# Optimization experiments

Measured on AMD Instinct MI355X. Metric: run time of the kernel, lower is better.

## Reference

```python
import jax, jax.numpy as jnp
import numpy as np

B, N, M = 2, 2048, 2048
D_K, D_V, H = 256, 256, 8
D_KS = D_K // H  # 32, per-head key dim (ceil(256/8))
D_VS = D_V // H  # 32
MASK_BIG = 1e32


def setup_inputs() -> dict:
    key = jax.random.key(0)
    ks = jax.random.split(key, 10)
    s = 0.02
    queries = jax.random.normal(ks[0], (B, N, D_K), jnp.float32)
    keys_ = jax.random.normal(ks[1], (B, M, D_K), jnp.float32)
    values = jax.random.normal(ks[2], (B, M, D_V), jnp.float32)
    presence = (jax.random.uniform(ks[3], (B, M)) > 0.3).astype(jnp.float32)
    Wq = jax.random.normal(ks[4], (D_K, D_KS * H), jnp.float32) * s
    bq = jnp.zeros((D_KS * H,), jnp.float32)
    Wk = jax.random.normal(ks[5], (D_K, D_KS * H), jnp.float32) * s
    bk = jnp.zeros((D_KS * H,), jnp.float32)
    Wv = jax.random.normal(ks[6], (D_V, D_VS * H), jnp.float32) * s
    bv = jnp.zeros((D_VS * H,), jnp.float32)
    Wo = jax.random.normal(ks[7], (D_VS * H, D_V), jnp.float32) * s
    bo = jnp.zeros((D_V,), jnp.float32)
    return {"queries": queries, "keys": keys_, "values": values, "presence": presence,
            "Wq": Wq, "bq": bq, "Wk": Wk, "bk": bk, "Wv": Wv, "bv": bv, "Wo": Wo, "bo": bo}


def reference(queries, keys, values, presence, Wq, bq, Wk, bk, Wv, bv, Wo, bo):
    # Project and split into heads. torch's split(d_k_s,-1)+cat(...,0) puts the
    # head index as the outer batch dim; a [B,N,H,d] reshape is the same math.
    q = (queries @ Wq + bq).reshape(B, N, H, D_KS)
    k = (keys @ Wk + bk).reshape(B, M, H, D_KS)
    v = (values @ Wv + bv).reshape(B, M, H, D_VS)
    # Raw scores, additive presence mask, then scale by sqrt(per-head d_k)
    scores = jnp.einsum('bnhd,bmhd->bhnm', q, k)
    scores = scores - (1.0 - presence)[:, None, None, :] * MASK_BIG
    attn = jax.nn.softmax(scores / np.sqrt(D_KS).astype(np.float32), axis=-1)
    o = jnp.einsum('bhnm,bmhd->bnhd', attn, v).reshape(B, N, H * D_VS)
    return o @ Wo + bo
```

## Files before the change

### kernel.cpp

```cpp
#include <hip/hip_runtime.h>

#define B_ 2
#define N_ 2048
#define M_ 2048
#define D_ 256
#define H_ 8
#define DH_ 32
#define SPLITS 2
#define QSCALE (0.17677669529663689f * 1.4426950408889634f)

typedef __attribute__((ext_vector_type(8))) short short8;
typedef __attribute__((ext_vector_type(4))) float f32x4;
typedef unsigned short u16;
typedef unsigned int u32;

#if __has_builtin(__builtin_amdgcn_exp2f)
#define EXP2 __builtin_amdgcn_exp2f
#else
#define EXP2 exp2f
#endif

__device__ __forceinline__ u16 f2bf(float f) {
  u32 u = __float_as_uint(f);
  return (u16)((u + 0x7fffu + ((u >> 16) & 1u)) >> 16);
}
__device__ __forceinline__ u32 cvtpk_bf16(float lo, float hi) {
  u32 r;
  asm("v_cvt_pk_bf16_f32 %0, %1, %2" : "=v"(r) : "v"(lo), "v"(hi));
  return r;
}
__device__ __forceinline__ void gload_lds16(const u16* g, u16* l) {
  __builtin_amdgcn_global_load_lds((const __attribute__((address_space(1))) void*)g,
                                   (__attribute__((address_space(3))) void*)l, 16, 0, 0);
}
__device__ __forceinline__ void gload_lds16f(const float* g, float* l) {
  __builtin_amdgcn_global_load_lds((const __attribute__((address_space(1))) void*)g,
                                   (__attribute__((address_space(3))) void*)l, 16, 0, 0);
}

__global__ __launch_bounds__(256) void wtconv_kernel(
    const float* __restrict__ Wq, const float* __restrict__ Wk,
    const float* __restrict__ Wv, const float* __restrict__ Wo,
    u16* __restrict__ wTq, u16* __restrict__ wTk, u16* __restrict__ wTv,
    u16* __restrict__ wTo) {
  __shared__ u16 sh[64][72];
  const int blk = blockIdx.x;
  const int mi = blk >> 4, tile = blk & 15;
  const float* Ws = mi == 0 ? Wq : mi == 1 ? Wk : mi == 2 ? Wv : Wo;
  u16* Wd = mi == 0 ? wTq : mi == 1 ? wTk : mi == 2 ? wTv : wTo;
  const int r0 = (tile >> 2) * 64, c0 = (tile & 3) * 64;
  const int r = threadIdx.x & 63, qt = threadIdx.x >> 6;
  const float* sp = Ws + (size_t)(r0 + r) * D_ + c0 + qt * 16;
  u32 w[8];
#pragma unroll
  for (int i = 0; i < 4; ++i) {
    f32x4 v = *(const f32x4*)(sp + i * 4);
    w[i * 2 + 0] = cvtpk_bf16(v[0], v[1]);
    w[i * 2 + 1] = cvtpk_bf16(v[2], v[3]);
  }
  *(uint4*)(&sh[r][qt * 16]) = *(uint4*)&w[0];
  *(uint4*)(&sh[r][qt * 16 + 8]) = *(uint4*)&w[4];
  __syncthreads();
  const int cc = threadIdx.x & 63;
  u32 t2[8];
#pragma unroll
  for (int i = 0; i < 8; ++i) {
    u32 lo = sh[qt * 16 + 2 * i][cc];
    u32 hi = sh[qt * 16 + 2 * i + 1][cc];
    t2[i] = lo | (hi << 16);
  }
  u16* op = Wd + (size_t)(c0 + cc) * D_ + r0 + qt * 16;
  *(uint4*)op = *(uint4*)&t2[0];
  *(uint4*)(op + 8) = *(uint4*)&t2[4];
}

__global__ __launch_bounds__(256, 4) void qkvproj_kernel(
    const float* __restrict__ Xq, const float* __restrict__ Xk, const float* __restrict__ Xv,
    const u16* __restrict__ wTq, const u16* __restrict__ wTk, const u16* __restrict__ wTv,
    const float* __restrict__ bq, const float* __restrict__ bk, const float* __restrict__ bv,
    u16* __restrict__ qb, u16* __restrict__ kb, u16* __restrict__ vtb) {
  __shared__ u16 xs[16 * 256];
  const int p = blockIdx.y;
  const int n0 = blockIdx.x * 16;
  const float* X = p == 0 ? Xq : (p == 1 ? Xk : Xv);
  const u16* wT = p == 0 ? wTq : (p == 1 ? wTk : wTv);
  const float* bias = p == 0 ? bq : (p == 1 ? bk : bv);
  const int t = threadIdx.x;

  {
    const int nL = t >> 4, kc = (t & 15) * 16;
    const float* xp = X + (size_t)(n0 + nL) * D_ + kc;
#pragma unroll
    for (int m = 0; m < 2; ++m) {
      const f32x4 a = *(const f32x4*)(xp + 8 * m);
      const f32x4 b2 = *(const f32x4*)(xp + 8 * m + 4);
      uint4 v;
      v.x = cvtpk_bf16(a[0], a[1]);
      v.y = cvtpk_bf16(a[2], a[3]);
      v.z = cvtpk_bf16(b2[0], b2[1]);
      v.w = cvtpk_bf16(b2[2], b2[3]);
      const int k0 = kc + 8 * m;
      *(uint4*)(xs + nL * 256 + (((k0 >> 3) ^ (nL & 7)) * 8)) = v;
    }
  }
  __syncthreads();

  const int wv = t >> 6, lane = t & 63, lr = lane & 15, lg = lane >> 4;
  const int c0 = wv * 64;
  const f32x4 zz = {0.f, 0.f, 0.f, 0.f};
  f32x4 acc[4] = {zz, zz, zz, zz};
#pragma unroll
  for (int ks = 0; ks < 8; ++ks) {
    const short8 a = *(const short8*)(xs + lr * 256 + (((ks * 4 + lg) ^ (lr & 7)) * 8));
#pragma unroll
    for (int ct = 0; ct < 4; ++ct) {
      const short8 b = *(const short8*)(wT + (size_t)(c0 + ct * 16 + lr) * D_ + ks * 32 + lg * 8);
      acc[ct] = __builtin_amdgcn_mfma_f32_16x16x32_bf16(a, b, acc[ct], 0, 0, 0);
    }
  }

  const int bidx = n0 >> 11;
  const int nn = (n0 & (N_ - 1)) + lg * 4;
  if (p < 2) {
    u16* ob = p == 0 ? qb : kb;
    const float sc = p == 0 ? QSCALE : 1.0f;
#pragma unroll
    for (int ct = 0; ct < 4; ++ct) {
      const int c = c0 + ct * 16 + lr;
      const float bb = bias[c];
      const int hh = c >> 5, dd = c & 31;
#pragma unroll
      for (int j = 0; j < 4; ++j)
        ob[((size_t)(bidx * H_ + hh) * N_ + nn + j) * DH_ + dd] =
            f2bf((acc[ct][j] + bb) * sc);
    }
  } else {
#pragma unroll
    for (int ct = 0; ct < 4; ++ct) {
      const int c = c0 + ct * 16 + lr;
      const float bb = bias[c];
      const int hh = c >> 5, dd = c & 31;
#pragma unroll
      for (int j = 0; j < 4; ++j)
        vtb[((size_t)(bidx * H_ + hh) * DH_ + dd) * M_ + nn + j] =
            f2bf(acc[ct][j] + bb);
    }
  }
}

__global__ __launch_bounds__(256, 4) void attn_kernel(
    const u16* __restrict__ qb, const u16* __restrict__ kb,
    const u16* __restrict__ vtb, const float* __restrict__ presence,
    float* __restrict__ opart, float* __restrict__ lpart) {
  __shared__ u16 kvlds[2][4096];
  __shared__ u16 plds[4][1024];
  __shared__ float prlds[1024];
  const int t = threadIdx.x;
  const int wv = t >> 6, lane = t & 63;
  const int lr = lane & 15, lg = lane >> 4;
  const int g = blockIdx.x;
  const int S = (g & 7) * 4 + ((g >> 3) & 3);
  const int qblk = g >> 5;
  const int s = S >> 4, bh = S & 15;
  const int b = bh >> 3, h = bh & 7;
  const int n0 = qblk * 64 + wv * 16;
  const int m0 = s * (M_ / SPLITS);
  const int NI = (M_ / SPLITS) / 64;

  const int gsk = (t & 3) ^ ((t >> 3) & 3);
  const u16* kst = kb + ((size_t)bh * M_ + m0 + (t >> 2)) * DH_ + gsk * 8;
  const int gsv = (t & 7) ^ ((t >> 3) & 7);
  const u16* vst = vtb + ((size_t)bh * DH_ + (t >> 3)) * M_ + m0 + gsv * 8;
  u16* const ldswK = &kvlds[0][0] + wv * 512;
  u16* const ldswV = &kvlds[0][0] + 2048 + wv * 512;

  const int ko0 = lr * 32 + (lg ^ ((lr >> 1) & 3)) * 8;
  const int sw = lr & 7;
  const int vo0 = (lg ^ sw) * 8;
  const int vo1 = ((4 + lg) ^ sw) * 8;

  const short8 qf = *(const short8*)(qb + ((size_t)bh * N_ + n0 + lr) * DH_ + lg * 8);
  u16* const plw = plds[wv] + lr * 64;

  const f32x4 zz = {0.f, 0.f, 0.f, 0.f};
  f32x4 o0 = zz, o1 = zz, racc = zz;

  gload_lds16(kst, ldswK);
  gload_lds16(vst, ldswV);
  gload_lds16f(presence + (size_t)b * M_ + m0 + wv * 256 + lane * 4, prlds + wv * 256);
  __syncthreads();

#pragma unroll 2
  for (int i = 0; i < NI; ++i) {
    const int mm = i * 64;
    const u16* kl = &kvlds[i & 1][0];
    const u16* vl = &kvlds[i & 1][2048];
    if (i + 1 < NI) {
      const int bo = ((i + 1) & 1) * 4096;
      gload_lds16(kst + (size_t)(i + 1) * (64 * DH_), ldswK + bo);
      gload_lds16(vst + (size_t)(i + 1) * 64, ldswV + bo);
    }

    f32x4 s4[4];
    __builtin_amdgcn_s_setprio(1);
#pragma unroll
    for (int tt = 0; tt < 4; ++tt) {
      const short8 kf = *(const short8*)(kl + tt * 512 + ko0);
      s4[tt] = __builtin_amdgcn_mfma_f32_16x16x32_bf16(kf, qf, zz, 0, 0, 0);
    }
    __builtin_amdgcn_s_setprio(0);

#pragma unroll
    for (int tt = 0; tt < 4; ++tt) {
      const f32x4 pr = *(const f32x4*)(prlds + mm + tt * 16 + lg * 4);
#pragma unroll
      for (int j = 0; j < 4; ++j) s4[tt][j] = EXP2(s4[tt][j]);
      s4[tt] *= pr;
      racc += s4[tt];
      const int slot = (2 * tt + (lg >> 1)) ^ sw;
      *(uint2*)(plw + slot * 8 + (lg & 1) * 4) =
          make_uint2(cvtpk_bf16(s4[tt][0], s4[tt][1]), cvtpk_bf16(s4[tt][2], s4[tt][3]));
    }
    const short8 pf0 = *(const short8*)(plw + vo0);
    const short8 pf1 = *(const short8*)(plw + vo1);
    const short8 vf0 = *(const short8*)(vl + lr * 64 + vo0);
    const short8 vf1 = *(const short8*)(vl + lr * 64 + vo1);
    const short8 vf2 = *(const short8*)(vl + (16 + lr) * 64 + vo0);
    const short8 vf3 = *(const short8*)(vl + (16 + lr) * 64 + vo1);
    __builtin_amdgcn_s_setprio(1);
    o0 = __builtin_amdgcn_mfma_f32_16x16x32_bf16(pf0, vf0, o0, 0, 0, 0);
    o0 = __builtin_amdgcn_mfma_f32_16x16x32_bf16(pf1, vf1, o0, 0, 0, 0);
    o1 = __builtin_amdgcn_mfma_f32_16x16x32_bf16(pf0, vf2, o1, 0, 0, 0);
    o1 = __builtin_amdgcn_mfma_f32_16x16x32_bf16(pf1, vf3, o1, 0, 0, 0);
    __builtin_amdgcn_s_setprio(0);
    __syncthreads();
  }

  float l = (racc[0] + racc[1]) + (racc[2] + racc[3]);
  l += __shfl_xor(l, 16);
  l += __shfl_xor(l, 32);
  if (lg == 0) lpart[((size_t)s * (B_ * N_) + b * N_ + n0 + lr) * H_ + h] = l;

  float* ob = opart + ((size_t)s * (B_ * N_) + (size_t)b * N_ + n0) * D_ + h * DH_;
#pragma unroll
  for (int j = 0; j < 4; ++j) {
    const int q = lg * 4 + j;
    ob[(size_t)q * D_ + lr] = o0[j];
    ob[(size_t)q * D_ + 16 + lr] = o1[j];
  }
}

__global__ __launch_bounds__(256, 4) void projo_kernel(
    const float* __restrict__ opart, const float* __restrict__ lpart,
    const u16* __restrict__ wTo, const float* __restrict__ bo,
    float* __restrict__ out) {
  __shared__ u16 xs[16 * 256];
  const int n0 = blockIdx.x * 16;
  const int t = threadIdx.x;

  {
    const int nL = t >> 4, kc = (t & 15) * 16;
    const int gn = n0 + nL;
    const float* o0p = opart + (size_t)gn * D_ + kc;
    const float* o1p = o0p + (size_t)(B_ * N_) * D_;
    const int h0 = kc >> 5;
    const float il = 1.f / (lpart[(size_t)gn * H_ + h0] +
                            lpart[((size_t)(B_ * N_) + gn) * H_ + h0]);
#pragma unroll
    for (int m = 0; m < 2; ++m) {
      f32x4 a = *(const f32x4*)(o0p + 8 * m) + *(const f32x4*)(o1p + 8 * m);
      f32x4 b2 = *(const f32x4*)(o0p + 8 * m + 4) + *(const f32x4*)(o1p + 8 * m + 4);
      a *= il;
      b2 *= il;
      uint4 v;
      v.x = cvtpk_bf16(a[0], a[1]);
      v.y = cvtpk_bf16(a[2], a[3]);
      v.z = cvtpk_bf16(b2[0], b2[1]);
      v.w = cvtpk_bf16(b2[2], b2[3]);
      const int k0 = kc + 8 * m;
      *(uint4*)(xs + nL * 256 + (((k0 >> 3) ^ (nL & 7)) * 8)) = v;
    }
  }
  __syncthreads();

  const int wv = t >> 6, lane = t & 63, lr = lane & 15, lg = lane >> 4;
  const int c0 = wv * 64;
  const f32x4 zz = {0.f, 0.f, 0.f, 0.f};
  f32x4 acc[4] = {zz, zz, zz, zz};
#pragma unroll
  for (int ks = 0; ks < 8; ++ks) {
    const short8 a = *(const short8*)(xs + lr * 256 + (((ks * 4 + lg) ^ (lr & 7)) * 8));
#pragma unroll
    for (int ct = 0; ct < 4; ++ct) {
      const short8 b = *(const short8*)(wTo + (size_t)(c0 + ct * 16 + lr) * D_ + ks * 32 + lg * 8);
      acc[ct] = __builtin_amdgcn_mfma_f32_16x16x32_bf16(a, b, acc[ct], 0, 0, 0);
    }
  }
#pragma unroll
  for (int ct = 0; ct < 4; ++ct) {
    const int c = c0 + ct * 16 + lr;
    const float bb = bo[c];
#pragma unroll
    for (int j = 0; j < 4; ++j)
      out[(size_t)(n0 + lg * 4 + j) * D_ + c] = acc[ct][j] + bb;
  }
}

extern "C" void kernel_launch(void* const* d_in, const int* in_sizes, int n_in,
                              void* d_out, int out_size, void* d_ws, size_t ws_size,
                              hipStream_t stream) {
  (void)in_sizes; (void)n_in; (void)out_size; (void)ws_size;
  const float* queries  = (const float*)d_in[0];
  const float* keys     = (const float*)d_in[1];
  const float* values   = (const float*)d_in[2];
  const float* presence = (const float*)d_in[3];
  const float* Wq = (const float*)d_in[4];
  const float* bq = (const float*)d_in[5];
  const float* Wk = (const float*)d_in[6];
  const float* bk = (const float*)d_in[7];
  const float* Wv = (const float*)d_in[8];
  const float* bv = (const float*)d_in[9];
  const float* Wo = (const float*)d_in[10];
  const float* bo = (const float*)d_in[11];

  u16* wTq = (u16*)d_ws;
  u16* wTk = wTq + 65536;
  u16* wTv = wTk + 65536;
  u16* wTo = wTv + 65536;
  u16* qb  = wTo + 65536;
  u16* kb  = qb + (size_t)B_ * H_ * N_ * DH_;
  u16* vtb = kb + (size_t)B_ * H_ * M_ * DH_;
  float* opart = (float*)(vtb + (size_t)B_ * H_ * DH_ * M_);
  float* lpart = opart + (size_t)SPLITS * B_ * N_ * D_;

  wtconv_kernel<<<64, 256, 0, stream>>>(Wq, Wk, Wv, Wo, wTq, wTk, wTv, wTo);
  qkvproj_kernel<<<dim3(256, 3), 256, 0, stream>>>(
      queries, keys, values, wTq, wTk, wTv, bq, bk, bv, qb, kb, vtb);
  attn_kernel<<<SPLITS * 16 * 32, 256, 0, stream>>>(qb, kb, vtb, presence, opart, lpart);
  projo_kernel<<<256, 256, 0, stream>>>(opart, lpart, wTo, bo, (float*)d_out);
}
```

Before: 54.63 us.

## Retile projection GEMMs with LDS-staged swizzled weights and simplify attention block mapping

Result: faster. 52.29 us (-4.3%).

```diff
diff --git a/kernel.cpp b/kernel.cpp
--- a/kernel.cpp
+++ b/kernel.cpp
@@ -69,29 +69,40 @@
     u32 hi = sh[qt * 16 + 2 * i + 1][cc];
     t2[i] = lo | (hi << 16);
   }
-  u16* op = Wd + (size_t)(c0 + cc) * D_ + r0 + qt * 16;
-  *(uint4*)op = *(uint4*)&t2[0];
-  *(uint4*)(op + 8) = *(uint4*)&t2[4];
-}
-
-__global__ __launch_bounds__(256, 4) void qkvproj_kernel(
+  const int crow = c0 + cc;
+  u16* rowb = Wd + (size_t)crow * D_;
+  const int sl0 = (r0 + qt * 16) >> 3;
+  *(uint4*)(rowb + ((sl0 ^ (crow & 7)) * 8)) = *(uint4*)&t2[0];
+  *(uint4*)(rowb + (((sl0 + 1) ^ (crow & 7)) * 8)) = *(uint4*)&t2[4];
+}
+
+__global__ __launch_bounds__(256, 3) void qkvproj_kernel(
     const float* __restrict__ Xq, const float* __restrict__ Xk, const float* __restrict__ Xv,
     const u16* __restrict__ wTq, const u16* __restrict__ wTk, const u16* __restrict__ wTv,
     const float* __restrict__ bq, const float* __restrict__ bk, const float* __restrict__ bv,
     u16* __restrict__ qb, u16* __restrict__ kb, u16* __restrict__ vtb) {
-  __shared__ u16 xs[16 * 256];
+  __shared__ u16 wsT[64 * 256];
+  __shared__ u16 xs[32 * 256];
   const int p = blockIdx.y;
-  const int n0 = blockIdx.x * 16;
+  const int nb = blockIdx.x & 127, cb = blockIdx.x >> 7;
+  const int n0B = nb * 32, c0B = cb * 64;
   const float* X = p == 0 ? Xq : (p == 1 ? Xk : Xv);
   const u16* wT = p == 0 ? wTq : (p == 1 ? wTk : wTv);
   const float* bias = p == 0 ? bq : (p == 1 ? bk : bv);
   const int t = threadIdx.x;
+  const int wv = t >> 6, lane = t & 63, lr = lane & 15, lg = lane >> 4;
 
   {
-    const int nL = t >> 4, kc = (t & 15) * 16;
-    const float* xp = X + (size_t)(n0 + nL) * D_ + kc;
-#pragma unroll
-    for (int m = 0; m < 2; ++m) {
+    const u16* wsrc = wT + (size_t)c0B * D_ + lane * 8;
+#pragma unroll
+    for (int i = 0; i < 8; ++i)
+      gload_lds16(wsrc + (wv * 8 + i) * 512, wsT + (wv * 8 + i) * 512);
+  }
+  {
+    const int nL = t >> 3, kc = (t & 7) * 32;
+    const float* xp = X + (size_t)(n0B + nL) * D_ + kc;
+#pragma unroll
+    for (int m = 0; m < 4; ++m) {
       const f32x4 a = *(const f32x4*)(xp + 8 * m);
       const f32x4 b2 = *(const f32x4*)(xp + 8 * m + 4);
       uint4 v;
@@ -105,45 +116,47 @@
   }
   __syncthreads();
 
-  const int wv = t >> 6, lane = t & 63, lr = lane & 15, lg = lane >> 4;
-  const int c0 = wv * 64;
   const f32x4 zz = {0.f, 0.f, 0.f, 0.f};
-  f32x4 acc[4] = {zz, zz, zz, zz};
+  f32x4 acc[2] = {zz, zz};
+  const int arow = wv * 16 + lr;
 #pragma unroll
   for (int ks = 0; ks < 8; ++ks) {
-    const short8 a = *(const short8*)(xs + lr * 256 + (((ks * 4 + lg) ^ (lr & 7)) * 8));
-#pragma unroll
-    for (int ct = 0; ct < 4; ++ct) {
-      const short8 b = *(const short8*)(wT + (size_t)(c0 + ct * 16 + lr) * D_ + ks * 32 + lg * 8);
-      acc[ct] = __builtin_amdgcn_mfma_f32_16x16x32_bf16(a, b, acc[ct], 0, 0, 0);
-    }
-  }
-
-  const int bidx = n0 >> 11;
-  const int nn = (n0 & (N_ - 1)) + lg * 4;
+    const short8 a = *(const short8*)(wsT + arow * 256 + (((ks * 4 + lg) ^ (arow & 7)) * 8));
+#pragma unroll
+    for (int ng = 0; ng < 2; ++ng) {
+      const int brow = ng * 16 + lr;
+      const short8 b = *(const short8*)(xs + brow * 256 + (((ks * 4 + lg) ^ (brow & 7)) * 8));
+      acc[ng] = __builtin_amdgcn_mfma_f32_16x16x32_bf16(a, b, acc[ng], 0, 0, 0);
+    }
+  }
+
+  const int cg4 = c0B + wv * 16 + lg * 4;
+  const f32x4 bias4 = *(const f32x4*)(bias + cg4);
   if (p < 2) {
     u16* ob = p == 0 ? qb : kb;
     const float sc = p == 0 ? QSCALE : 1.0f;
 #pragma unroll
-    for (int ct = 0; ct < 4; ++ct) {
-      const int c = c0 + ct * 16 + lr;
-      const float bb = bias[c];
-      const int hh = c >> 5, dd = c & 31;
-#pragma unroll
-      for (int j = 0; j < 4; ++j)
-        ob[((size_t)(bidx * H_ + hh) * N_ + nn + j) * DH_ + dd] =
-            f2bf((acc[ct][j] + bb) * sc);
+    for (int ng = 0; ng < 2; ++ng) {
+      const int n = n0B + ng * 16 + lr;
+      const int b = n >> 11, nn = n & (N_ - 1);
+#pragma unroll
+      for (int j = 0; j < 4; ++j) {
+        const int c = cg4 + j;
+        ob[((size_t)(b * H_ + (c >> 5)) * N_ + nn) * DH_ + (c & 31)] =
+            f2bf((acc[ng][j] + bias4[j]) * sc);
+      }
     }
   } else {
 #pragma unroll
-    for (int ct = 0; ct < 4; ++ct) {
-      const int c = c0 + ct * 16 + lr;
-      const float bb = bias[c];
-      const int hh = c >> 5, dd = c & 31;
-#pragma unroll
-      for (int j = 0; j < 4; ++j)
-        vtb[((size_t)(bidx * H_ + hh) * DH_ + dd) * M_ + nn + j] =
-            f2bf(acc[ct][j] + bb);
+    for (int ng = 0; ng < 2; ++ng) {
+      const int n = n0B + ng * 16 + lr;
+      const int b = n >> 11, nn = n & (M_ - 1);
+#pragma unroll
+      for (int j = 0; j < 4; ++j) {
+        const int c = cg4 + j;
+        vtb[((size_t)(b * H_ + (c >> 5)) * DH_ + (c & 31)) * M_ + nn] =
+            f2bf(acc[ng][j] + bias4[j]);
+      }
     }
   }
 }
@@ -158,10 +171,9 @@
   const int t = threadIdx.x;
   const int wv = t >> 6, lane = t & 63;
   const int lr = lane & 15, lg = lane >> 4;
-  const int g = blockIdx.x;
-  const int S = (g & 7) * 4 + ((g >> 3) & 3);
-  const int qblk = g >> 5;
-  const int s = S >> 4, bh = S & 15;
+  const int s = blockIdx.x >> 9;
+  const int bh = (blockIdx.x >> 5) & 15;
+  const int qblk = blockIdx.x & 31;
   const int b = bh >> 3, h = bh & 7;
   const int n0 = qblk * 64 + wv * 16;
   const int m0 = s * (M_ / SPLITS);
@@ -250,24 +262,33 @@
   }
 }
 
-__global__ __launch_bounds__(256, 4) void projo_kernel(
+__global__ __launch_bounds__(256, 3) void projo_kernel(
     const float* __restrict__ opart, const float* __restrict__ lpart,
     const u16* __restrict__ wTo, const float* __restrict__ bo,
     float* __restrict__ out) {
-  __shared__ u16 xs[16 * 256];
-  const int n0 = blockIdx.x * 16;
+  __shared__ u16 ws[64 * 256];
+  __shared__ u16 xs[32 * 256];
+  const int nb = blockIdx.x & 127, cb = blockIdx.x >> 7;
+  const int n0B = nb * 32, c0B = cb * 64;
   const int t = threadIdx.x;
+  const int wv = t >> 6, lane = t & 63, lr = lane & 15, lg = lane >> 4;
 
   {
-    const int nL = t >> 4, kc = (t & 15) * 16;
-    const int gn = n0 + nL;
+    const u16* wsrc = wTo + (size_t)c0B * D_ + lane * 8;
+#pragma unroll
+    for (int i = 0; i < 8; ++i)
+      gload_lds16(wsrc + (wv * 8 + i) * 512, ws + (wv * 8 + i) * 512);
+  }
+  {
+    const int nL = t >> 3, kc = (t & 7) * 32;
+    const int gn = n0B + nL;
     const float* o0p = opart + (size_t)gn * D_ + kc;
     const float* o1p = o0p + (size_t)(B_ * N_) * D_;
     const int h0 = kc >> 5;
     const float il = 1.f / (lpart[(size_t)gn * H_ + h0] +
                             lpart[((size_t)(B_ * N_) + gn) * H_ + h0]);
 #pragma unroll
-    for (int m = 0; m < 2; ++m) {
+    for (int m = 0; m < 4; ++m) {
       f32x4 a = *(const f32x4*)(o0p + 8 * m) + *(const f32x4*)(o1p + 8 * m);
       f32x4 b2 = *(const f32x4*)(o0p + 8 * m + 4) + *(const f32x4*)(o1p + 8 * m + 4);
       a *= il;
@@ -283,26 +304,27 @@
   }
   __syncthreads();
 
-  const int wv = t >> 6, lane = t & 63, lr = lane & 15, lg = lane >> 4;
-  const int c0 = wv * 64;
   const f32x4 zz = {0.f, 0.f, 0.f, 0.f};
-  f32x4 acc[4] = {zz, zz, zz, zz};
+  f32x4 acc[2] = {zz, zz};
+  const int arow = (wv & 1) * 16 + lr;
+  const int cw0 = (wv >> 1) * 32;
 #pragma unroll
   for (int ks = 0; ks < 8; ++ks) {
-    const short8 a = *(const short8*)(xs + lr * 256 + (((ks * 4 + lg) ^ (lr & 7)) * 8));
-#pragma unroll
-    for (int ct = 0; ct < 4; ++ct) {
-      const short8 b = *(const short8*)(wTo + (size_t)(c0 + ct * 16 + lr) * D_ + ks * 32 + lg * 8);
-      acc[ct] = __builtin_amdgcn_mfma_f32_16x16x32_bf16(a, b, acc[ct], 0, 0, 0);
-    }
-  }
-#pragma unroll
-  for (int ct = 0; ct < 4; ++ct) {
-    const int c = c0 + ct * 16 + lr;
+    const short8 a = *(const short8*)(xs + arow * 256 + (((ks * 4 + lg) ^ (arow & 7)) * 8));
+#pragma unroll
+    for (int ng = 0; ng < 2; ++ng) {
+      const int brow = cw0 + ng * 16 + lr;
+      const short8 b = *(const short8*)(ws + brow * 256 + (((ks * 4 + lg) ^ (brow & 7)) * 8));
+      acc[ng] = __builtin_amdgcn_mfma_f32_16x16x32_bf16(a, b, acc[ng], 0, 0, 0);
+    }
+  }
+#pragma unroll
+  for (int ng = 0; ng < 2; ++ng) {
+    const int c = c0B + cw0 + ng * 16 + lr;
     const float bb = bo[c];
 #pragma unroll
     for (int j = 0; j < 4; ++j)
-      out[(size_t)(n0 + lg * 4 + j) * D_ + c] = acc[ct][j] + bb;
+      out[(size_t)(n0B + (wv & 1) * 16 + lg * 4 + j) * D_ + c] = acc[ng][j] + bb;
   }
 }
 
@@ -334,8 +356,8 @@
   float* lpart = opart + (size_t)SPLITS * B_ * N_ * D_;
 
   wtconv_kernel<<<64, 256, 0, stream>>>(Wq, Wk, Wv, Wo, wTq, wTk, wTv, wTo);
-  qkvproj_kernel<<<dim3(256, 3), 256, 0, stream>>>(
+  qkvproj_kernel<<<dim3(512, 3), 256, 0, stream>>>(
       queries, keys, values, wTq, wTk, wTv, bq, bk, bv, qb, kb, vtb);
   attn_kernel<<<SPLITS * 16 * 32, 256, 0, stream>>>(qb, kb, vtb, presence, opart, lpart);
-  projo_kernel<<<256, 256, 0, stream>>>(opart, lpart, wTo, bo, (float*)d_out);
-}
+  projo_kernel<<<512, 256, 0, stream>>>(opart, lpart, wTo, bo, (float*)d_out);
+}
```
